# Kernel optimization log

Measured on AMD Instinct MI355X. Metric: run time of the kernel, lower is better.

## Reference

```python
import jax, jax.numpy as jnp
import numpy as np

B, T, J, D = 128, 256, 50, 3
I, H, C = J * D, 1024, 60


def setup_inputs() -> dict:
    key = jax.random.key(0)
    ks = jax.random.split(key, 10)
    s = 0.02
    return {
        "x": jax.random.normal(ks[0], (B, T, J, D), dtype=jnp.float32),
        "h1": jnp.zeros((B, H), jnp.float32),
        "c1": jnp.zeros((B, H), jnp.float32),
        "h2": jnp.zeros((B, H), jnp.float32),
        "c2": jnp.zeros((B, H), jnp.float32),
        "W_ih1": jax.random.normal(ks[1], (4 * H, I), jnp.float32) * s,
        "W_hh1": jax.random.normal(ks[2], (4 * H, H), jnp.float32) * s,
        "b_ih1": jax.random.normal(ks[3], (4 * H,), jnp.float32) * s,
        "b_hh1": jax.random.normal(ks[4], (4 * H,), jnp.float32) * s,
        "W_ih2": jax.random.normal(ks[5], (4 * H, H), jnp.float32) * s,
        "W_hh2": jax.random.normal(ks[6], (4 * H, H), jnp.float32) * s,
        "b_ih2": jax.random.normal(ks[7], (4 * H,), jnp.float32) * s,
        "b_hh2": jax.random.normal(ks[8], (4 * H,), jnp.float32) * s,
        "W_fc": jax.random.normal(ks[9], (C, H), jnp.float32) * s,
        "b_fc": jnp.zeros((C,), jnp.float32),
        "mode": 0,  # 0 == 'val' (no dropout), static
    }


def _lstm_cell(xv, h, c, Wih, Whh, bih, bhh):
    # PyTorch LSTMCell gate order: i, f, g, o
    gates = xv @ Wih.T + bih + h @ Whh.T + bhh  # [B, 4H]
    i, f, g, o = jnp.split(gates, 4, axis=-1)
    c_new = jax.nn.sigmoid(f) * c + jax.nn.sigmoid(i) * jnp.tanh(g)
    h_new = jax.nn.sigmoid(o) * jnp.tanh(c_new)
    return h_new, c_new


def reference(x, h1, c1, h2, c2, W_ih1, W_hh1, b_ih1, b_hh1,
              W_ih2, W_hh2, b_ih2, b_hh2, W_fc, b_fc, mode):
    b, t = x.shape[0], x.shape[1]
    xs = x.reshape(b, t, -1).transpose(1, 0, 2)  # [T, B, I]

    def step(carry, xt):
        h1, c1, h2, c2 = carry
        h1, c1 = _lstm_cell(xt, h1, c1, W_ih1, W_hh1, b_ih1, b_hh1)
        # mode==0 ('val'): no dropout between layers
        h2, c2 = _lstm_cell(h1, h2, c2, W_ih2, W_hh2, b_ih2, b_hh2)
        return (h1, c1, h2, c2), None

    (h1, c1, h2, c2), _ = jax.lax.scan(step, (h1, c1, h2, c2), xs)
    return h2 @ W_fc.T + b_fc  # [B, num_class]
```

## Files before the change

### kernel.cpp

```cpp
#include <hip/hip_runtime.h>
#include <math.h>


typedef __bf16 bf16;
typedef __bf16 bf16x8 __attribute__((ext_vector_type(8)));
typedef float floatx4 __attribute__((ext_vector_type(4)));
typedef unsigned long long ull;

#define B_   128
#define T_   256
#define H_   1024
#define I_   150
#define KX_  160
#define C_   60
#define K1LDS 1280
#define KP    1024
#define K2LDS 2048
#define NLINES 32
#define CSTRIDE 64
#define FLAGLINE 16
#define NCOLS 32
#define NHC  8
#define NT   2

template<int N> struct IC { static constexpr int value = N; };

__device__ __forceinline__ float sigmoidf_(float x) { return 1.f / (1.f + expf(-x)); }

__global__ __launch_bounds__(256)
void convert_all(const float* __restrict__ x,
                 const float* __restrict__ h1in, const float* __restrict__ h2in,
                 bf16* __restrict__ xb, bf16* __restrict__ h1b0, bf16* __restrict__ h2b0,
                 unsigned* __restrict__ cnt)
{
    const size_t nXB = (size_t)T_ * B_ * KX_;
    const size_t nHC = (size_t)B_ * H_;
    size_t idx = (size_t)blockIdx.x * 256 + threadIdx.x;

    if (idx < nXB) {
        size_t t = idx / (B_ * KX_);
        size_t r = idx - t * (B_ * KX_);
        size_t b = r / KX_, k = r - b * KX_;
        xb[idx] = (k < I_) ? (bf16)x[(b * T_ + t) * I_ + k] : (bf16)0.f;
        return;
    }
    idx -= nXB;
    if (idx < nHC) { h1b0[idx] = (bf16)h1in[idx]; return; }
    idx -= nHC;
    if (idx < nHC) { h2b0[idx] = (bf16)h2in[idx]; return; }
    idx -= nHC;
    if (idx < NLINES * CSTRIDE) cnt[idx] = 0u;
}

__global__ __launch_bounds__(512, 2)
void rnn_rebal8(const bf16* __restrict__ xb,
                bf16* __restrict__ h1b0, bf16* __restrict__ h1b1,
                bf16* __restrict__ h2b0, bf16* __restrict__ h2b1,
                float* __restrict__ p0, float* __restrict__ p1,
                const float* __restrict__ c1in, const float* __restrict__ c2in,
                const float* __restrict__ Wih1, const float* __restrict__ Whh1,
                const float* __restrict__ bih1, const float* __restrict__ bhh1,
                const float* __restrict__ Wih2, const float* __restrict__ Whh2,
                const float* __restrict__ bih2, const float* __restrict__ bhh2,
                const float* __restrict__ Wfc, const float* __restrict__ bfc,
                float* __restrict__ out, unsigned* __restrict__ cnt, int nblk)
{
    extern __shared__ bf16 lds[];
    __shared__ __align__(16) bf16 hst[8][16][NHC];

    const int tid   = threadIdx.x;
    const int bid   = blockIdx.x;
    const int layer = (bid >> 3) & 1;
    const int slice = (bid & 7) | ((bid >> 4) << 3);
    const int n0h   = slice * NHC;
    const int arr_per_line = nblk >> 4;
    bf16* ldsP = lds + 32 * K1LDS;

    if (layer == 0) {
        {
            const int cpr = K1LDS >> 3;
            const int total = NCOLS * cpr;
            for (int ci = tid; ci < total; ci += 512) {
                int r = ci / cpr, c = ci - r * cpr;
                int g = r / NHC, j = r - g * NHC;
                int grow = (g << 10) + n0h + j;
                int k0 = c << 3;
                float v[8];
#pragma unroll
                for (int u = 0; u < 8; ++u) {
                    int k = k0 + u;
                    v[u] = (k < I_) ? Wih1[(size_t)grow * I_ + k]
                         : (k < KX_) ? 0.f
                         : (k < KX_ + H_) ? Whh1[(size_t)grow * H_ + (k - KX_)] : 0.f;
                }
                int cs = (c & ~15) | ((c ^ r) & 15);
                bf16* dst = lds + (size_t)r * K1LDS + (cs << 3);
#pragma unroll
                for (int u = 0; u < 8; ++u) dst[u] = (bf16)v[u];
            }
        }
        {
            const int cpr = KP >> 3;
            const int total = NCOLS * cpr;
            for (int ci = tid; ci < total; ci += 512) {
                int r = ci / cpr, c = ci - r * cpr;
                int g = r / NHC, j = r - g * NHC;
                int grow = (g << 10) + n0h + j;
                int k0 = c << 3;
                float v[8];
#pragma unroll
                for (int u = 0; u < 8; ++u) v[u] = Wih2[(size_t)grow * H_ + k0 + u];
                int cs = (c & ~15) | ((c ^ r) & 15);
                bf16* dst = ldsP + (size_t)r * KP + (cs << 3);
#pragma unroll
                for (int u = 0; u < 8; ++u) dst[u] = (bf16)v[u];
            }
        }
    } else {
        const int cpr = KP >> 3;
        const int total = NCOLS * cpr;
        for (int ci = tid; ci < total; ci += 512) {
            int r = ci / cpr, c = ci - r * cpr;
            int g = r / NHC, j = r - g * NHC;
            int grow = (g << 10) + n0h + j;
            int k0 = c << 3;
            float v[8];
#pragma unroll
            for (int u = 0; u < 8; ++u) v[u] = Whh2[(size_t)grow * H_ + k0 + u];
            int cs = (c & ~15) | ((c ^ r) & 15);
            bf16* dst = lds + (size_t)r * KP + (cs << 3);
#pragma unroll
            for (int u = 0; u < 8; ++u) dst[u] = (bf16)v[u];
        }
    }
    __syncthreads();

    const int lane = tid & 63;
    const int wv   = tid >> 6;
    const int jj   = lane & (NHC - 1);
    const int quad = lane >> 4;

    float4 bias;
    {
        const float* bi = layer ? bih2 : bih1;
        const float* bh = layer ? bhh2 : bhh1;
        int col = n0h + jj;
        bias.x = bi[col] + bh[col];
        bias.y = bi[col + H_] + bh[col + H_];
        bias.z = bi[col + 2 * H_] + bh[col + 2 * H_];
        bias.w = bi[col + 3 * H_] + bh[col + 3 * H_];
    }

    float creg[2];
    {
        const float* cin = layer ? c2in : c1in;
        int dup = (lane >> 3) & 1;
#pragma unroll
        for (int rp = 0; rp < 2; ++rp) {
            int row = wv * 16 + quad * 4 + rp * 2 + dup;
            creg[rp] = cin[(size_t)row * H_ + n0h + jj];
        }
    }

    floatx4 acc[NT];
    floatx4 pacc[NT];

    auto seg1 = [&](const bf16* A, int ldA, const bf16* Bb, int ldB,
                    auto nksC, int ksBase) {
        constexpr int NKS = decltype(nksC)::value;
        constexpr int CH  = NKS < 16 ? NKS : 16;
        const int arow = wv * 16 + (lane & 15);
        const bf16* a0 = A + (size_t)arow * ldA + quad * 8;
        for (int blk = 0; blk < NKS; blk += CH) {
            bf16x8 a0r[CH];
#pragma unroll
            for (int i = 0; i < CH; ++i)
                a0r[i] = *(const bf16x8*)(a0 + (blk + i) * 32);
            __builtin_amdgcn_sched_barrier(0);
#pragma unroll
            for (int i = 0; i < CH; ++i) {
                int c = (ksBase + blk + i) * 4 + quad;
#pragma unroll
                for (int t = 0; t < NT; ++t) {
                    int r = t * 16 + (lane & 15);
                    int cs = (c & ~15) | ((c ^ r) & 15);
                    bf16x8 bfr = *(const bf16x8*)(Bb + (size_t)r * ldB + (cs << 3));
                    acc[t] = __builtin_amdgcn_mfma_f32_16x16x32_bf16(a0r[i], bfr, acc[t], 0, 0, 0);
                }
            }
        }
    };

    auto segDual = [&](const bf16* A) {
        const int arow = wv * 16 + (lane & 15);
        const bf16* a0 = A + (size_t)arow * H_ + quad * 8;
        for (int blk = 0; blk < 32; blk += 16) {
            bf16x8 a0r[16];
#pragma unroll
            for (int i = 0; i < 16; ++i)
                a0r[i] = *(const bf16x8*)(a0 + (blk + i) * 32);
            __builtin_amdgcn_sched_barrier(0);
#pragma unroll
            for (int i = 0; i < 16; ++i) {
                int ig = blk + i;
                int c1 = (5 + ig) * 4 + quad;
                int cp = ig * 4 + quad;
#pragma unroll
                for (int t = 0; t < NT; ++t) {
                    int r = t * 16 + (lane & 15);
                    int cs1 = (c1 & ~15) | ((c1 ^ r) & 15);
                    bf16x8 b1 = *(const bf16x8*)(lds + (size_t)r * K1LDS + (cs1 << 3));
                    acc[t] = __builtin_amdgcn_mfma_f32_16x16x32_bf16(a0r[i], b1, acc[t], 0, 0, 0);
                    int csp = (cp & ~15) | ((cp ^ r) & 15);
                    bf16x8 bp = *(const bf16x8*)(ldsP + (size_t)r * KP + (csp << 3));
                    pacc[t] = __builtin_amdgcn_mfma_f32_16x16x32_bf16(a0r[i], bp, pacc[t], 0, 0, 0);
                }
            }
        }
    };

    auto epilogue = [&](bf16* hw) {
        const int base = lane & 48;
#pragma unroll
        for (int r = 0; r < 4; ++r) {
            float vi = __shfl(acc[0][r], base + jj, 64);
            float vf = __shfl(acc[0][r], base + 8 + jj, 64);
            float vg = __shfl(acc[1][r], base + jj, 64);
            float vo = __shfl(acc[1][r], base + 8 + jj, 64);
            bool cond = (((lane >> 3) & 1) == (r & 1));
            int slot = r >> 1;
            if (cond) {
                float cv = creg[slot];
                float cn = sigmoidf_(vf + bias.y) * cv
                         + sigmoidf_(vi + bias.x) * tanhf(vg + bias.z);
                creg[slot] = cn;
                float hn = sigmoidf_(vo + bias.w) * tanhf(cn);
                hst[wv][quad * 4 + r][jj] = (bf16)hn;
            }
        }
        __syncthreads();
        if (lane < 32) {
            int row_l = lane >> 1, cg = lane & 1;
            ull v = *(const ull*)&hst[wv][row_l][cg * 4];
            __hip_atomic_store((ull*)(hw + (size_t)(wv * 16 + row_l) * H_ + n0h + cg * 4),
                               v, __ATOMIC_RELAXED, __HIP_MEMORY_SCOPE_AGENT);
        }
    };

    if (layer == 0) {
#pragma unroll
        for (int t = 0; t < NT; ++t) {
            acc[t]  = (floatx4){0.f, 0.f, 0.f, 0.f};
            pacc[t] = (floatx4){0.f, 0.f, 0.f, 0.f};
        }
        seg1(xb, KX_, lds, K1LDS, IC<5>{}, 0);
    }

    for (int e = 0; e <= T_ + 1; ++e) {
        if (layer == 0 && e <= T_) {
            const bf16* h1r = (e & 1) ? h1b1 : h1b0;
            segDual(h1r);

            float* pw = ((e & 1) ? p1 : p0) + (size_t)slice * B_ * NCOLS;
#pragma unroll
            for (int t = 0; t < NT; ++t)
#pragma unroll
                for (int r = 0; r < 4; ++r) {
                    int row = wv * 16 + quad * 4 + r;
                    __hip_atomic_store(pw + (size_t)row * NCOLS + t * 16 + (lane & 15),
                                       pacc[t][r], __ATOMIC_RELAXED, __HIP_MEMORY_SCOPE_AGENT);
                }

            if (e < T_) {
                bf16* hw = (e & 1) ? h1b0 : h1b1;
                epilogue(hw);
            }
        } else if (layer == 1 && e >= 2) {
#pragma unroll
            for (int t = 0; t < NT; ++t) acc[t] = (floatx4){0.f, 0.f, 0.f, 0.f};

            const float* pr = ((e & 1) ? p0 : p1) + (size_t)slice * B_ * NCOLS;
            float pv[NT][4];
#pragma unroll
            for (int t = 0; t < NT; ++t)
#pragma unroll
                for (int r = 0; r < 4; ++r) {
                    int row = wv * 16 + quad * 4 + r;
                    pv[t][r] = pr[(size_t)row * NCOLS + t * 16 + (lane & 15)];
                }

            const bf16* h2r = (e & 1) ? h2b1 : h2b0;
            seg1(h2r, H_, lds, KP, IC<32>{}, 0);

#pragma unroll
            for (int t = 0; t < NT; ++t)
#pragma unroll
                for (int r = 0; r < 4; ++r) acc[t][r] += pv[t][r];

            bf16* hw = (e & 1) ? h2b0 : h2b1;
            epilogue(hw);
        }

        asm volatile("s_waitcnt vmcnt(0)" ::: "memory");
        __syncthreads();
        const unsigned etag = (unsigned)(e + 1);
        if (tid == 0)
            __hip_atomic_fetch_add(cnt + (bid & 15) * CSTRIDE, 1u,
                                   __ATOMIC_RELAXED, __HIP_MEMORY_SCOPE_AGENT);
        if (layer == 0 && e < T_) {
#pragma unroll
            for (int t = 0; t < NT; ++t) {
                acc[t]  = (floatx4){0.f, 0.f, 0.f, 0.f};
                pacc[t] = (floatx4){0.f, 0.f, 0.f, 0.f};
            }
            if (e + 1 < T_)
                seg1(xb + (size_t)(e + 1) * B_ * KX_, KX_, lds, K1LDS, IC<5>{}, 0);
        }
        if (bid == 0) {
            if (tid < 16) {
                const unsigned tgt = etag * (unsigned)arr_per_line;
                const unsigned* cp = cnt + tid * CSTRIDE;
                while (__hip_atomic_load(cp, __ATOMIC_RELAXED, __HIP_MEMORY_SCOPE_AGENT) < tgt)
                    __builtin_amdgcn_s_sleep(1);
            }
            if (tid == 0)
                __hip_atomic_store(cnt + FLAGLINE * CSTRIDE, etag,
                                   __ATOMIC_RELAXED, __HIP_MEMORY_SCOPE_AGENT);
        } else {
            if (tid == 0) {
                const unsigned* fp = cnt + FLAGLINE * CSTRIDE;
                while (__hip_atomic_load(fp, __ATOMIC_RELAXED, __HIP_MEMORY_SCOPE_AGENT) < etag)
                    __builtin_amdgcn_s_sleep(1);
            }
        }
        __syncthreads();
        if (tid < 64)
            __builtin_amdgcn_fence(__ATOMIC_ACQUIRE, "agent");
        __syncthreads();
    }

    if (bid < B_) {
        const bf16* h2f = h2b0;
        for (int c = wv; c < C_; c += 8) {
            float a = 0.f;
            for (int k = lane; k < H_; k += 64)
                a += (float)h2f[(size_t)bid * H_ + k] * Wfc[(size_t)c * H_ + k];
#pragma unroll
            for (int off = 32; off; off >>= 1) a += __shfl_down(a, off, 64);
            if (lane == 0) out[bid * C_ + c] = a + bfc[c];
        }
    }
}

__global__ __launch_bounds__(512, 2)
void rnn_fallback8(const bf16* __restrict__ xb,
                   bf16* __restrict__ h1b0, bf16* __restrict__ h1b1,
                   bf16* __restrict__ h2b0, bf16* __restrict__ h2b1,
                   float* __restrict__ p0, float* __restrict__ p1,
                   const float* __restrict__ c1in, const float* __restrict__ c2in,
                   const float* __restrict__ Wih1, const float* __restrict__ Whh1,
                   const float* __restrict__ bih1, const float* __restrict__ bhh1,
                   const float* __restrict__ Wih2, const float* __restrict__ Whh2,
                   const float* __restrict__ bih2, const float* __restrict__ bhh2,
                   const float* __restrict__ Wfc, const float* __restrict__ bfc,
                   float* __restrict__ out, unsigned* __restrict__ cnt, int nblk)
{
    extern __shared__ bf16 lds[];
    __shared__ __align__(16) bf16 hst[8][16][NHC];

    const int tid   = threadIdx.x;
    const int bid   = blockIdx.x;
    const int layer = (bid >> 3) & 1;
    const int slice = (bid & 7) | ((bid >> 4) << 3);
    const int n0h   = slice * NHC;
    const int KLDS  = layer ? K2LDS : K1LDS;
    const int arr_per_line = nblk >> 3;

    {
        const int cpr = KLDS >> 3;
        const int total = NCOLS * cpr;
        for (int ci = tid; ci < total; ci += 512) {
            int r = ci / cpr, c = ci - r * cpr;
            int g = r / NHC, j = r - g * NHC;
            int grow = (g << 10) + n0h + j;
            int k0 = c << 3;
            float v[8];
#pragma unroll
            for (int u = 0; u < 8; ++u) {
                int k = k0 + u;
                if (layer == 0)
                    v[u] = (k < I_) ? Wih1[(size_t)grow * I_ + k]
                         : (k < KX_) ? 0.f
                         : (k < KX_ + H_) ? Whh1[(size_t)grow * H_ + (k - KX_)] : 0.f;
                else
                    v[u] = (k < H_) ? Wih2[(size_t)grow * H_ + k]
                                    : Whh2[(size_t)grow * H_ + (k - H_)];
            }
            int cs = (c & ~15) | ((c ^ r) & 15);
            bf16* dst = lds + (size_t)r * KLDS + (cs << 3);
#pragma unroll
            for (int u = 0; u < 8; ++u) dst[u] = (bf16)v[u];
        }
    }
    __syncthreads();

    const int lane = tid & 63;
    const int wv   = tid >> 6;
    const int jj   = lane & (NHC - 1);
    const int quad = lane >> 4;

    float4 bias;
    {
        const float* bi = layer ? bih2 : bih1;
        const float* bh = layer ? bhh2 : bhh1;
        int col = n0h + jj;
        bias.x = bi[col] + bh[col];
        bias.y = bi[col + H_] + bh[col + H_];
        bias.z = bi[col + 2 * H_] + bh[col + 2 * H_];
        bias.w = bi[col + 3 * H_] + bh[col + 3 * H_];
    }

    float creg[2];
    {
        const float* cin = layer ? c2in : c1in;
        int dup = (lane >> 3) & 1;
#pragma unroll
        for (int rp = 0; rp < 2; ++rp) {
            int row = wv * 16 + quad * 4 + rp * 2 + dup;
            creg[rp] = cin[(size_t)row * H_ + n0h + jj];
        }
    }

    floatx4 acc[NT];

    auto seg = [&](const bf16* A, int ldA, auto nksC, int ksBase) {
        constexpr int NKS = decltype(nksC)::value;
        constexpr int CH  = NKS < 16 ? NKS : 16;
        const int arow = wv * 16 + (lane & 15);
        const bf16* a0 = A + (size_t)arow * ldA + quad * 8;
        for (int blk = 0; blk < NKS; blk += CH) {
            bf16x8 a0r[CH];
#pragma unroll
            for (int i = 0; i < CH; ++i)
                a0r[i] = *(const bf16x8*)(a0 + (blk + i) * 32);
            __builtin_amdgcn_sched_barrier(0);
#pragma unroll
            for (int i = 0; i < CH; ++i) {
                int c = (ksBase + blk + i) * 4 + quad;
#pragma unroll
                for (int t = 0; t < NT; ++t) {
                    int r = t * 16 + (lane & 15);
                    int cs = (c & ~15) | ((c ^ r) & 15);
                    bf16x8 bfr = *(const bf16x8*)(lds + (size_t)r * KLDS + (cs << 3));
                    acc[t] = __builtin_amdgcn_mfma_f32_16x16x32_bf16(a0r[i], bfr, acc[t], 0, 0, 0);
                }
            }
        }
    };

    for (int e = 0; e <= T_; ++e) {
        const bool active = layer == 0 ? (e < T_) : (e >= 1);
        if (active) {
#pragma unroll
            for (int t = 0; t < NT; ++t) acc[t] = (floatx4){0.f, 0.f, 0.f, 0.f};

            const bf16* h1r = (e & 1) ? h1b1 : h1b0;
            if (layer == 0) {
                const bf16* xt = xb + (size_t)e * B_ * KX_;
                seg(xt, KX_, IC<5>{}, 0);
                seg(h1r, H_, IC<32>{}, 5);
            } else {
                const bf16* h2r = (e & 1) ? h2b0 : h2b1;
                seg(h1r, H_, IC<32>{}, 0);
                seg(h2r, H_, IC<32>{}, 32);
            }
            bf16* hw = (layer == 0) ? ((e & 1) ? h1b0 : h1b1)
                                    : ((e & 1) ? h2b1 : h2b0);

            const int base = lane & 48;
#pragma unroll
            for (int r = 0; r < 4; ++r) {
                float vi = __shfl(acc[0][r], base + jj, 64);
                float vf = __shfl(acc[0][r], base + 8 + jj, 64);
                float vg = __shfl(acc[1][r], base + jj, 64);
                float vo = __shfl(acc[1][r], base + 8 + jj, 64);
                bool cond = (((lane >> 3) & 1) == (r & 1));
                int slot = r >> 1;
                if (cond) {
                    float cv = creg[slot];
                    float cn = sigmoidf_(vf + bias.y) * cv
                             + sigmoidf_(vi + bias.x) * tanhf(vg + bias.z);
                    creg[slot] = cn;
                    float hn = sigmoidf_(vo + bias.w) * tanhf(cn);
                    hst[wv][quad * 4 + r][jj] = (bf16)hn;
                }
            }
            __syncthreads();
            if (lane < 32) {
                int row_l = lane >> 1, cg = lane & 1;
                ull v = *(const ull*)&hst[wv][row_l][cg * 4];
                __hip_atomic_store((ull*)(hw + (size_t)(wv * 16 + row_l) * H_ + n0h + cg * 4),
                                   v, __ATOMIC_RELAXED, __HIP_MEMORY_SCOPE_AGENT);
            }
        }

        asm volatile("s_waitcnt vmcnt(0)" ::: "memory");
        __syncthreads();
        const unsigned etag = (unsigned)(e + 1);
        if (bid == 0) {
            if (tid == 0)
                __hip_atomic_fetch_add(cnt, 1u, __ATOMIC_RELAXED, __HIP_MEMORY_SCOPE_AGENT);
            if (tid < 8) {
                const unsigned tgt = etag * (unsigned)arr_per_line;
                const unsigned* cp = cnt + tid * CSTRIDE;
                while (__hip_atomic_load(cp, __ATOMIC_RELAXED, __HIP_MEMORY_SCOPE_AGENT) < tgt)
                    __builtin_amdgcn_s_sleep(1);
            }
            if (tid == 0)
                __hip_atomic_store(cnt + 8 * CSTRIDE, etag,
                                   __ATOMIC_RELAXED, __HIP_MEMORY_SCOPE_AGENT);
        } else {
            if (tid == 0) {
                __hip_atomic_fetch_add(cnt + (bid & 7) * CSTRIDE, 1u,
                                       __ATOMIC_RELAXED, __HIP_MEMORY_SCOPE_AGENT);
                const unsigned* fp = cnt + 8 * CSTRIDE;
                while (__hip_atomic_load(fp, __ATOMIC_RELAXED, __HIP_MEMORY_SCOPE_AGENT) < etag)
                    __builtin_amdgcn_s_sleep(1);
            }
        }
        __syncthreads();
        if (tid < 64)
            __builtin_amdgcn_fence(__ATOMIC_ACQUIRE, "agent");
        __syncthreads();
    }

    if (bid < B_) {
        const bf16* h2f = h2b0;
        for (int c = wv; c < C_; c += 8) {
            float a = 0.f;
            for (int k = lane; k < H_; k += 64)
                a += (float)h2f[(size_t)bid * H_ + k] * Wfc[(size_t)c * H_ + k];
#pragma unroll
            for (int off = 32; off; off >>= 1) a += __shfl_down(a, off, 64);
            if (lane == 0) out[bid * C_ + c] = a + bfc[c];
        }
    }
}

extern "C" void kernel_launch(void* const* d_in, const int* in_sizes, int n_in,
                              void* d_out, int out_size, void* d_ws, size_t ws_size,
                              hipStream_t stream)
{
    const float* x    = (const float*)d_in[0];
    const float* h1in = (const float*)d_in[1];
    const float* c1in = (const float*)d_in[2];
    const float* h2in = (const float*)d_in[3];
    const float* c2in = (const float*)d_in[4];
    const float* Wih1 = (const float*)d_in[5];
    const float* Whh1 = (const float*)d_in[6];
    const float* bih1 = (const float*)d_in[7];
    const float* bhh1 = (const float*)d_in[8];
    const float* Wih2 = (const float*)d_in[9];
    const float* Whh2 = (const float*)d_in[10];
    const float* bih2 = (const float*)d_in[11];
    const float* bhh2 = (const float*)d_in[12];
    const float* Wfc  = (const float*)d_in[13];
    const float* bfc  = (const float*)d_in[14];
    float* out = (float*)d_out;

    const size_t szXB  = (size_t)T_ * B_ * KX_ * 2;
    const size_t szH   = (size_t)B_ * H_ * 2;
    const size_t szCnt = (size_t)NLINES * CSTRIDE * 4;
    const size_t szP   = (size_t)128 * B_ * NCOLS * 4;
    const size_t needBase  = szXB + 4 * szH + szCnt;
    const size_t needRebal = needBase + 2 * szP;

    char* p = (char*)d_ws;
    bf16* xb = (bf16*)p;    p += szXB;
    bf16* h1b0 = (bf16*)p;  p += szH;
    bf16* h1b1 = (bf16*)p;  p += szH;
    bf16* h2b0 = (bf16*)p;  p += szH;
    bf16* h2b1 = (bf16*)p;  p += szH;
    unsigned* cnt = (unsigned*)p;  p += szCnt;
    float* p0 = (float*)p;  p += szP;
    float* p1 = (float*)p;

    const size_t citems = (size_t)T_ * B_ * KX_ + 2 * (size_t)B_ * H_ + NLINES * CSTRIDE;
    convert_all<<<(int)((citems + 255) / 256), 256, 0, stream>>>(
        x, h1in, h2in, xb, h1b0, h2b0, cnt);

    int nblk = 256;
    void* args[] = { &xb, &h1b0, &h1b1, &h2b0, &h2b1, &p0, &p1,
                     (void*)&c1in, (void*)&c2in,
                     (void*)&Wih1, (void*)&Whh1, (void*)&bih1, (void*)&bhh1,
                     (void*)&Wih2, (void*)&Whh2, (void*)&bih2, (void*)&bhh2,
                     (void*)&Wfc, (void*)&bfc, &out, &cnt, &nblk };

    hipError_t err = hipErrorOutOfMemory;
    if (ws_size >= needRebal) {
        const unsigned ldsRebal = (unsigned)(32 * K1LDS + 32 * KP) * 2u;
        if (hipFuncSetAttribute((const void*)rnn_rebal8,
                                hipFuncAttributeMaxDynamicSharedMemorySize,
                                (int)ldsRebal) == hipSuccess) {
            err = hipLaunchCooperativeKernel((const void*)rnn_rebal8,
                                             dim3(256), dim3(512), args,
                                             ldsRebal, stream);
        }
    }
    if (err != hipSuccess) {
        (void)hipGetLastError();
        (void)hipFuncSetAttribute((const void*)rnn_fallback8,
                                  hipFuncAttributeMaxDynamicSharedMemorySize, 131072);
        (void)hipLaunchCooperativeKernel((const void*)rnn_fallback8,
                                         dim3(256), dim3(512), args,
                                         131072u, stream);
    }
}
```

Before: 3.548 ms.

## Replace per-step acquire fence with relaxed atomic loads of shared state

Removes the per-timestep agent-scope acquire fence and the extra barrier in the persistent recurrence loop. Instead, cross-block hidden-state and partial-sum reads use relaxed agent-scope atomic loads so they bypass stale caches, with a single fence kept before the final FC. The aim is to cut the cache invalidation and barrier cost on every step of the grid-wide sync. The risk is that 8-byte atomic loads replace 16-byte vector loads, and that ordering now relies on relaxed atomics without an explicit acquire.

```diff
diff --git a/kernel.cpp b/kernel.cpp
--- a/kernel.cpp
+++ b/kernel.cpp
@@ -27,6 +27,15 @@
 
 __device__ __forceinline__ float sigmoidf_(float x) { return 1.f / (1.f + expf(-x)); }
 
+union U16B { ull u[2]; bf16x8 v; };
+
+__device__ __forceinline__ bf16x8 loadH16(const bf16* p) {
+    U16B x;
+    x.u[0] = __hip_atomic_load((const ull*)p,     __ATOMIC_RELAXED, __HIP_MEMORY_SCOPE_AGENT);
+    x.u[1] = __hip_atomic_load((const ull*)p + 1, __ATOMIC_RELAXED, __HIP_MEMORY_SCOPE_AGENT);
+    return x.v;
+}
+
 __global__ __launch_bounds__(256)
 void convert_all(const float* __restrict__ x,
                  const float* __restrict__ h1in, const float* __restrict__ h2in,
@@ -165,26 +174,44 @@
     floatx4 acc[NT];
     floatx4 pacc[NT];
 
-    auto seg1 = [&](const bf16* A, int ldA, const bf16* Bb, int ldB,
-                    auto nksC, int ksBase) {
-        constexpr int NKS = decltype(nksC)::value;
-        constexpr int CH  = NKS < 16 ? NKS : 16;
+    auto segX = [&](const bf16* A) {
         const int arow = wv * 16 + (lane & 15);
-        const bf16* a0 = A + (size_t)arow * ldA + quad * 8;
-        for (int blk = 0; blk < NKS; blk += CH) {
-            bf16x8 a0r[CH];
-#pragma unroll
-            for (int i = 0; i < CH; ++i)
-                a0r[i] = *(const bf16x8*)(a0 + (blk + i) * 32);
+        const bf16* a0 = A + (size_t)arow * KX_ + quad * 8;
+        bf16x8 a0r[5];
+#pragma unroll
+        for (int i = 0; i < 5; ++i)
+            a0r[i] = *(const bf16x8*)(a0 + i * 32);
+        __builtin_amdgcn_sched_barrier(0);
+#pragma unroll
+        for (int i = 0; i < 5; ++i) {
+            int c = i * 4 + quad;
+#pragma unroll
+            for (int t = 0; t < NT; ++t) {
+                int r = t * 16 + (lane & 15);
+                int cs = (c & ~15) | ((c ^ r) & 15);
+                bf16x8 bfr = *(const bf16x8*)(lds + (size_t)r * K1LDS + (cs << 3));
+                acc[t] = __builtin_amdgcn_mfma_f32_16x16x32_bf16(a0r[i], bfr, acc[t], 0, 0, 0);
+            }
+        }
+    };
+
+    auto segH2 = [&](const bf16* A) {
+        const int arow = wv * 16 + (lane & 15);
+        const bf16* a0 = A + (size_t)arow * H_ + quad * 8;
+        for (int blk = 0; blk < 32; blk += 16) {
+            bf16x8 a0r[16];
+#pragma unroll
+            for (int i = 0; i < 16; ++i)
+                a0r[i] = loadH16(a0 + (blk + i) * 32);
             __builtin_amdgcn_sched_barrier(0);
 #pragma unroll
-            for (int i = 0; i < CH; ++i) {
-                int c = (ksBase + blk + i) * 4 + quad;
+            for (int i = 0; i < 16; ++i) {
+                int c = (blk + i) * 4 + quad;
 #pragma unroll
                 for (int t = 0; t < NT; ++t) {
                     int r = t * 16 + (lane & 15);
                     int cs = (c & ~15) | ((c ^ r) & 15);
-                    bf16x8 bfr = *(const bf16x8*)(Bb + (size_t)r * ldB + (cs << 3));
+                    bf16x8 bfr = *(const bf16x8*)(lds + (size_t)r * KP + (cs << 3));
                     acc[t] = __builtin_amdgcn_mfma_f32_16x16x32_bf16(a0r[i], bfr, acc[t], 0, 0, 0);
                 }
             }
@@ -198,7 +225,7 @@
             bf16x8 a0r[16];
 #pragma unroll
             for (int i = 0; i < 16; ++i)
-                a0r[i] = *(const bf16x8*)(a0 + (blk + i) * 32);
+                a0r[i] = loadH16(a0 + (blk + i) * 32);
             __builtin_amdgcn_sched_barrier(0);
 #pragma unroll
             for (int i = 0; i < 16; ++i) {
@@ -253,7 +280,7 @@
             acc[t]  = (floatx4){0.f, 0.f, 0.f, 0.f};
             pacc[t] = (floatx4){0.f, 0.f, 0.f, 0.f};
         }
-        seg1(xb, KX_, lds, K1LDS, IC<5>{}, 0);
+        segX(xb);
     }
 
     for (int e = 0; e <= T_ + 1; ++e) {
@@ -286,11 +313,12 @@
 #pragma unroll
                 for (int r = 0; r < 4; ++r) {
                     int row = wv * 16 + quad * 4 + r;
-                    pv[t][r] = pr[(size_t)row * NCOLS + t * 16 + (lane & 15)];
+                    pv[t][r] = __hip_atomic_load(pr + (size_t)row * NCOLS + t * 16 + (lane & 15),
+                                                 __ATOMIC_RELAXED, __HIP_MEMORY_SCOPE_AGENT);
                 }
 
             const bf16* h2r = (e & 1) ? h2b1 : h2b0;
-            seg1(h2r, H_, lds, KP, IC<32>{}, 0);
+            segH2(h2r);
 
 #pragma unroll
             for (int t = 0; t < NT; ++t)
@@ -314,7 +342,7 @@
                 pacc[t] = (floatx4){0.f, 0.f, 0.f, 0.f};
             }
             if (e + 1 < T_)
-                seg1(xb + (size_t)(e + 1) * B_ * KX_, KX_, lds, K1LDS, IC<5>{}, 0);
+                segX(xb + (size_t)(e + 1) * B_ * KX_);
         }
         if (bid == 0) {
             if (tid < 16) {
@@ -334,10 +362,11 @@
             }
         }
         __syncthreads();
-        if (tid < 64)
-            __builtin_amdgcn_fence(__ATOMIC_ACQUIRE, "agent");
-        __syncthreads();
-    }
+    }
+
+    if (tid < 64)
+        __builtin_amdgcn_fence(__ATOMIC_ACQUIRE, "agent");
+    __syncthreads();
 
     if (bid < B_) {
         const bf16* h2f = h2b0;
```

Result: slower. 4.864 ms (+37.1%).

## Decouple layer barriers with per-layer flags and triple-buffered partials

Applied to the files above, without the earlier changes.

Adds a new persistent kernel in which layer-0 and layer-1 blocks synchronize through separate barrier flags instead of one global barrier each step. The partial-product buffer becomes triple-buffered, so layer 0 can run up to two steps ahead of layer 1, and layer-1 blocks wait only on their own layer plus layer 0's progress. This is meant to shrink the critical path of the grid-wide barrier and let the layers overlap. In exchange it needs more workspace and more complex cross-layer dependency logic, and it drops the old fallback kernel.

```diff
diff --git a/kernel.cpp b/kernel.cpp
--- a/kernel.cpp
+++ b/kernel.cpp
@@ -15,10 +15,11 @@
 #define C_   60
 #define K1LDS 1280
 #define KP    1024
-#define K2LDS 2048
-#define NLINES 32
+#define NLINES 40
 #define CSTRIDE 64
 #define FLAGLINE 16
+#define L0FLAG 32
+#define L1FLAG 33
 #define NCOLS 32
 #define NHC  8
 #define NT   2
@@ -50,6 +51,353 @@
     if (idx < nHC) { h2b0[idx] = (bf16)h2in[idx]; return; }
     idx -= nHC;
     if (idx < NLINES * CSTRIDE) cnt[idx] = 0u;
+}
+
+__device__ __forceinline__ void stage_rebal(
+    bf16* lds, bf16* ldsP, int tid, int layer, int n0h,
+    const float* Wih1, const float* Whh1, const float* Wih2, const float* Whh2)
+{
+    if (layer == 0) {
+        {
+            const int cpr = K1LDS >> 3;
+            const int total = NCOLS * cpr;
+            for (int ci = tid; ci < total; ci += 512) {
+                int r = ci / cpr, c = ci - r * cpr;
+                int g = r / NHC, j = r - g * NHC;
+                int grow = (g << 10) + n0h + j;
+                int k0 = c << 3;
+                float v[8];
+#pragma unroll
+                for (int u = 0; u < 8; ++u) {
+                    int k = k0 + u;
+                    v[u] = (k < I_) ? Wih1[(size_t)grow * I_ + k]
+                         : (k < KX_) ? 0.f
+                         : (k < KX_ + H_) ? Whh1[(size_t)grow * H_ + (k - KX_)] : 0.f;
+                }
+                int cs = (c & ~15) | ((c ^ r) & 15);
+                bf16* dst = lds + (size_t)r * K1LDS + (cs << 3);
+#pragma unroll
+                for (int u = 0; u < 8; ++u) dst[u] = (bf16)v[u];
+            }
+        }
+        {
+            const int cpr = KP >> 3;
+            const int total = NCOLS * cpr;
+            for (int ci = tid; ci < total; ci += 512) {
+                int r = ci / cpr, c = ci - r * cpr;
+                int g = r / NHC, j = r - g * NHC;
+                int grow = (g << 10) + n0h + j;
+                int k0 = c << 3;
+                float v[8];
+#pragma unroll
+                for (int u = 0; u < 8; ++u) v[u] = Wih2[(size_t)grow * H_ + k0 + u];
+                int cs = (c & ~15) | ((c ^ r) & 15);
+                bf16* dst = ldsP + (size_t)r * KP + (cs << 3);
+#pragma unroll
+                for (int u = 0; u < 8; ++u) dst[u] = (bf16)v[u];
+            }
+        }
+    } else {
+        const int cpr = KP >> 3;
+        const int total = NCOLS * cpr;
+        for (int ci = tid; ci < total; ci += 512) {
+            int r = ci / cpr, c = ci - r * cpr;
+            int g = r / NHC, j = r - g * NHC;
+            int grow = (g << 10) + n0h + j;
+            int k0 = c << 3;
+            float v[8];
+#pragma unroll
+            for (int u = 0; u < 8; ++u) v[u] = Whh2[(size_t)grow * H_ + k0 + u];
+            int cs = (c & ~15) | ((c ^ r) & 15);
+            bf16* dst = lds + (size_t)r * KP + (cs << 3);
+#pragma unroll
+            for (int u = 0; u < 8; ++u) dst[u] = (bf16)v[u];
+        }
+    }
+}
+
+__global__ __launch_bounds__(512, 2)
+void rnn_decoup8(const bf16* __restrict__ xb,
+                 bf16* __restrict__ h1b0, bf16* __restrict__ h1b1,
+                 bf16* __restrict__ h2b0, bf16* __restrict__ h2b1,
+                 float* __restrict__ p0, float* __restrict__ p1, float* __restrict__ p2,
+                 const float* __restrict__ c1in, const float* __restrict__ c2in,
+                 const float* __restrict__ Wih1, const float* __restrict__ Whh1,
+                 const float* __restrict__ bih1, const float* __restrict__ bhh1,
+                 const float* __restrict__ Wih2, const float* __restrict__ Whh2,
+                 const float* __restrict__ bih2, const float* __restrict__ bhh2,
+                 const float* __restrict__ Wfc, const float* __restrict__ bfc,
+                 float* __restrict__ out, unsigned* __restrict__ cnt, int nblk)
+{
+    extern __shared__ bf16 lds[];
+    __shared__ __align__(16) bf16 hst[8][16][NHC];
+
+    const int tid   = threadIdx.x;
+    const int bid   = blockIdx.x;
+    const int layer = (bid >> 3) & 1;
+    const int slice = (bid & 7) | ((bid >> 4) << 3);
+    const int n0h   = slice * NHC;
+    const int line  = layer * 16 + ((bid & 7) | (((bid >> 4) & 1) << 3));
+    bf16* ldsP = lds + 32 * K1LDS;
+
+    stage_rebal(lds, ldsP, tid, layer, n0h, Wih1, Whh1, Wih2, Whh2);
+    __syncthreads();
+
+    const int lane = tid & 63;
+    const int wv   = tid >> 6;
+    const int jj   = lane & (NHC - 1);
+    const int quad = lane >> 4;
+
+    float4 bias;
+    {
+        const float* bi = layer ? bih2 : bih1;
+        const float* bh = layer ? bhh2 : bhh1;
+        int col = n0h + jj;
+        bias.x = bi[col] + bh[col];
+        bias.y = bi[col + H_] + bh[col + H_];
+        bias.z = bi[col + 2 * H_] + bh[col + 2 * H_];
+        bias.w = bi[col + 3 * H_] + bh[col + 3 * H_];
+    }
+
+    float creg[2];
+    {
+        const float* cin = layer ? c2in : c1in;
+        int dup = (lane >> 3) & 1;
+#pragma unroll
+        for (int rp = 0; rp < 2; ++rp) {
+            int row = wv * 16 + quad * 4 + rp * 2 + dup;
+            creg[rp] = cin[(size_t)row * H_ + n0h + jj];
+        }
+    }
+
+    floatx4 acc[NT];
+    floatx4 pacc[NT];
+
+    auto seg1 = [&](const bf16* A, int ldA, const bf16* Bb, int ldB,
+                    auto nksC, int ksBase) {
+        constexpr int NKS = decltype(nksC)::value;
+        constexpr int CH  = NKS < 16 ? NKS : 16;
+        const int arow = wv * 16 + (lane & 15);
+        const bf16* a0 = A + (size_t)arow * ldA + quad * 8;
+        for (int blk = 0; blk < NKS; blk += CH) {
+            bf16x8 a0r[CH];
+#pragma unroll
+            for (int i = 0; i < CH; ++i)
+                a0r[i] = *(const bf16x8*)(a0 + (blk + i) * 32);
+            __builtin_amdgcn_sched_barrier(0);
+#pragma unroll
+            for (int i = 0; i < CH; ++i) {
+                int c = (ksBase + blk + i) * 4 + quad;
+#pragma unroll
+                for (int t = 0; t < NT; ++t) {
+                    int r = t * 16 + (lane & 15);
+                    int cs = (c & ~15) | ((c ^ r) & 15);
+                    bf16x8 bfr = *(const bf16x8*)(Bb + (size_t)r * ldB + (cs << 3));
+                    acc[t] = __builtin_amdgcn_mfma_f32_16x16x32_bf16(a0r[i], bfr, acc[t], 0, 0, 0);
+                }
+            }
+        }
+    };
+
+    auto segDual = [&](const bf16* A) {
+        const int arow = wv * 16 + (lane & 15);
+        const bf16* a0 = A + (size_t)arow * H_ + quad * 8;
+        for (int blk = 0; blk < 32; blk += 16) {
+            bf16x8 a0r[16];
+#pragma unroll
+            for (int i = 0; i < 16; ++i)
+                a0r[i] = *(const bf16x8*)(a0 + (blk + i) * 32);
+            __builtin_amdgcn_sched_barrier(0);
+#pragma unroll
+            for (int i = 0; i < 16; ++i) {
+                int ig = blk + i;
+                int c1 = (5 + ig) * 4 + quad;
+                int cp = ig * 4 + quad;
+#pragma unroll
+                for (int t = 0; t < NT; ++t) {
+                    int r = t * 16 + (lane & 15);
+                    int cs1 = (c1 & ~15) | ((c1 ^ r) & 15);
+                    bf16x8 b1 = *(const bf16x8*)(lds + (size_t)r * K1LDS + (cs1 << 3));
+                    acc[t] = __builtin_amdgcn_mfma_f32_16x16x32_bf16(a0r[i], b1, acc[t], 0, 0, 0);
+                    int csp = (cp & ~15) | ((cp ^ r) & 15);
+                    bf16x8 bp = *(const bf16x8*)(ldsP + (size_t)r * KP + (csp << 3));
+                    pacc[t] = __builtin_amdgcn_mfma_f32_16x16x32_bf16(a0r[i], bp, pacc[t], 0, 0, 0);
+                }
+            }
+        }
+    };
+
+    auto epilogue = [&](bf16* hw) {
+        const int base = lane & 48;
+#pragma unroll
+        for (int r = 0; r < 4; ++r) {
+            float vi = __shfl(acc[0][r], base + jj, 64);
+            float vf = __shfl(acc[0][r], base + 8 + jj, 64);
+            float vg = __shfl(acc[1][r], base + jj, 64);
+            float vo = __shfl(acc[1][r], base + 8 + jj, 64);
+            bool cond = (((lane >> 3) & 1) == (r & 1));
+            int slot = r >> 1;
+            if (cond) {
+                float cv = creg[slot];
+                float cn = sigmoidf_(vf + bias.y) * cv
+                         + sigmoidf_(vi + bias.x) * tanhf(vg + bias.z);
+                creg[slot] = cn;
+                float hn = sigmoidf_(vo + bias.w) * tanhf(cn);
+                hst[wv][quad * 4 + r][jj] = (bf16)hn;
+            }
+        }
+        __syncthreads();
+        if (lane < 32) {
+            int row_l = lane >> 1, cg = lane & 1;
+            ull v = *(const ull*)&hst[wv][row_l][cg * 4];
+            __hip_atomic_store((ull*)(hw + (size_t)(wv * 16 + row_l) * H_ + n0h + cg * 4),
+                               v, __ATOMIC_RELAXED, __HIP_MEMORY_SCOPE_AGENT);
+        }
+    };
+
+    if (layer == 0) {
+#pragma unroll
+        for (int t = 0; t < NT; ++t) {
+            acc[t]  = (floatx4){0.f, 0.f, 0.f, 0.f};
+            pacc[t] = (floatx4){0.f, 0.f, 0.f, 0.f};
+        }
+        seg1(xb, KX_, lds, K1LDS, IC<5>{}, 0);
+    }
+
+    for (int e = 0; e <= T_ + 1; ++e) {
+        const int pm  = e % 3;
+        const int pmr = (e + 2) % 3;
+        float* const pbuf[3] = { p0, p1, p2 };
+
+        if (layer == 0 && e <= T_) {
+            const bf16* h1r = (e & 1) ? h1b1 : h1b0;
+            segDual(h1r);
+
+            float* pw = pbuf[pm] + (size_t)slice * B_ * NCOLS;
+#pragma unroll
+            for (int t = 0; t < NT; ++t)
+#pragma unroll
+                for (int r = 0; r < 4; ++r) {
+                    int row = wv * 16 + quad * 4 + r;
+                    __hip_atomic_store(pw + (size_t)row * NCOLS + t * 16 + (lane & 15),
+                                       pacc[t][r], __ATOMIC_RELAXED, __HIP_MEMORY_SCOPE_AGENT);
+                }
+
+            if (e < T_) {
+                bf16* hw = (e & 1) ? h1b0 : h1b1;
+                epilogue(hw);
+            }
+        } else if (layer == 1 && e >= 2) {
+#pragma unroll
+            for (int t = 0; t < NT; ++t) acc[t] = (floatx4){0.f, 0.f, 0.f, 0.f};
+
+            const float* pr = pbuf[pmr] + (size_t)slice * B_ * NCOLS;
+            float pv[NT][4];
+#pragma unroll
+            for (int t = 0; t < NT; ++t)
+#pragma unroll
+                for (int r = 0; r < 4; ++r) {
+                    int row = wv * 16 + quad * 4 + r;
+                    pv[t][r] = pr[(size_t)row * NCOLS + t * 16 + (lane & 15)];
+                }
+
+            const bf16* h2r = (e & 1) ? h2b1 : h2b0;
+            seg1(h2r, H_, lds, KP, IC<32>{}, 0);
+
+#pragma unroll
+            for (int t = 0; t < NT; ++t)
+#pragma unroll
+                for (int r = 0; r < 4; ++r) acc[t][r] += pv[t][r];
+
+            bf16* hw = (e & 1) ? h2b0 : h2b1;
+            epilogue(hw);
+        }
+
+        asm volatile("s_waitcnt vmcnt(0)" ::: "memory");
+        __syncthreads();
+        const int etag = e + 1;
+        if (tid == 0)
+            __hip_atomic_fetch_add(cnt + line * CSTRIDE, 1u,
+                                   __ATOMIC_RELAXED, __HIP_MEMORY_SCOPE_AGENT);
+        if (layer == 0 && e < T_) {
+#pragma unroll
+            for (int t = 0; t < NT; ++t) {
+                acc[t]  = (floatx4){0.f, 0.f, 0.f, 0.f};
+                pacc[t] = (floatx4){0.f, 0.f, 0.f, 0.f};
+            }
+            if (e + 1 < T_)
+                seg1(xb + (size_t)(e + 1) * B_ * KX_, KX_, lds, K1LDS, IC<5>{}, 0);
+        }
+        if (layer == 0) {
+            if (bid == 0) {
+                if (tid < 16) {
+                    const unsigned tgt = 8u * (unsigned)etag;
+                    const unsigned* cp = cnt + tid * CSTRIDE;
+                    while (__hip_atomic_load(cp, __ATOMIC_RELAXED, __HIP_MEMORY_SCOPE_AGENT) < tgt)
+                        __builtin_amdgcn_s_sleep(1);
+                }
+                if (tid == 0)
+                    __hip_atomic_store(cnt + L0FLAG * CSTRIDE, (unsigned)etag,
+                                       __ATOMIC_RELAXED, __HIP_MEMORY_SCOPE_AGENT);
+            } else if (tid == 0) {
+                const unsigned* fp = cnt + L0FLAG * CSTRIDE;
+                while (__hip_atomic_load(fp, __ATOMIC_RELAXED, __HIP_MEMORY_SCOPE_AGENT) < (unsigned)etag)
+                    __builtin_amdgcn_s_sleep(1);
+            }
+            if (tid == 0 && etag >= 3) {
+                const unsigned* fp = cnt + L1FLAG * CSTRIDE;
+                while (__hip_atomic_load(fp, __ATOMIC_RELAXED, __HIP_MEMORY_SCOPE_AGENT) < (unsigned)(etag - 2))
+                    __builtin_amdgcn_s_sleep(1);
+            }
+        } else {
+            if (bid == 8) {
+                if (tid < 16) {
+                    const unsigned tgt = 8u * (unsigned)etag;
+                    const unsigned* cp = cnt + (16 + tid) * CSTRIDE;
+                    while (__hip_atomic_load(cp, __ATOMIC_RELAXED, __HIP_MEMORY_SCOPE_AGENT) < tgt)
+                        __builtin_amdgcn_s_sleep(1);
+                }
+                if (tid == 0)
+                    __hip_atomic_store(cnt + L1FLAG * CSTRIDE, (unsigned)etag,
+                                       __ATOMIC_RELAXED, __HIP_MEMORY_SCOPE_AGENT);
+            } else if (tid == 0) {
+                const unsigned* fp = cnt + L1FLAG * CSTRIDE;
+                while (__hip_atomic_load(fp, __ATOMIC_RELAXED, __HIP_MEMORY_SCOPE_AGENT) < (unsigned)etag)
+                    __builtin_amdgcn_s_sleep(1);
+            }
+            if (tid == 0) {
+                const unsigned* fp = cnt + L0FLAG * CSTRIDE;
+                while (__hip_atomic_load(fp, __ATOMIC_RELAXED, __HIP_MEMORY_SCOPE_AGENT) < (unsigned)etag)
+                    __builtin_amdgcn_s_sleep(1);
+            }
+        }
+        __syncthreads();
+        if (tid < 64)
+            __builtin_amdgcn_fence(__ATOMIC_ACQUIRE, "agent");
+        __syncthreads();
+    }
+
+    if (tid == 0 && layer == 0) {
+        const unsigned* fp = cnt + L1FLAG * CSTRIDE;
+        while (__hip_atomic_load(fp, __ATOMIC_RELAXED, __HIP_MEMORY_SCOPE_AGENT) < (unsigned)(T_ + 2))
+            __builtin_amdgcn_s_sleep(1);
+    }
+    __syncthreads();
+    if (tid < 64)
+        __builtin_amdgcn_fence(__ATOMIC_ACQUIRE, "agent");
+    __syncthreads();
+
+    if (bid < B_) {
+        const bf16* h2f = h2b0;
+        for (int c = wv; c < C_; c += 8) {
+            float a = 0.f;
+            for (int k = lane; k < H_; k += 64)
+                a += (float)h2f[(size_t)bid * H_ + k] * Wfc[(size_t)c * H_ + k];
+#pragma unroll
+            for (int off = 32; off; off >>= 1) a += __shfl_down(a, off, 64);
+            if (lane == 0) out[bid * C_ + c] = a + bfc[c];
+        }
+    }
 }
 
 __global__ __launch_bounds__(512, 2)
@@ -76,63 +424,7 @@
     const int arr_per_line = nblk >> 4;
     bf16* ldsP = lds + 32 * K1LDS;
 
-    if (layer == 0) {
-        {
-            const int cpr = K1LDS >> 3;
-            const int total = NCOLS * cpr;
-            for (int ci = tid; ci < total; ci += 512) {
-                int r = ci / cpr, c = ci - r * cpr;
-                int g = r / NHC, j = r - g * NHC;
-                int grow = (g << 10) + n0h + j;
-                int k0 = c << 3;
-                float v[8];
-#pragma unroll
-                for (int u = 0; u < 8; ++u) {
-                    int k = k0 + u;
-                    v[u] = (k < I_) ? Wih1[(size_t)grow * I_ + k]
-                         : (k < KX_) ? 0.f
-                         : (k < KX_ + H_) ? Whh1[(size_t)grow * H_ + (k - KX_)] : 0.f;
-                }
-                int cs = (c & ~15) | ((c ^ r) & 15);
-                bf16* dst = lds + (size_t)r * K1LDS + (cs << 3);
-#pragma unroll
-                for (int u = 0; u < 8; ++u) dst[u] = (bf16)v[u];
-            }
-        }
-        {
-            const int cpr = KP >> 3;
-            const int total = NCOLS * cpr;
-            for (int ci = tid; ci < total; ci += 512) {
-                int r = ci / cpr, c = ci - r * cpr;
-                int g = r / NHC, j = r - g * NHC;
-                int grow = (g << 10) + n0h + j;
-                int k0 = c << 3;
-                float v[8];
-#pragma unroll
-                for (int u = 0; u < 8; ++u) v[u] = Wih2[(size_t)grow * H_ + k0 + u];
-                int cs = (c & ~15) | ((c ^ r) & 15);
-                bf16* dst = ldsP + (size_t)r * KP + (cs << 3);
-#pragma unroll
-                for (int u = 0; u < 8; ++u) dst[u] = (bf16)v[u];
-            }
-        }
-    } else {
-        const int cpr = KP >> 3;
-        const int total = NCOLS * cpr;
-        for (int ci = tid; ci < total; ci += 512) {
-            int r = ci / cpr, c = ci - r * cpr;
-            int g = r / NHC, j = r - g * NHC;
-            int grow = (g << 10) + n0h + j;
-            int k0 = c << 3;
-            float v[8];
-#pragma unroll
-            for (int u = 0; u < 8; ++u) v[u] = Whh2[(size_t)grow * H_ + k0 + u];
-            int cs = (c & ~15) | ((c ^ r) & 15);
-            bf16* dst = lds + (size_t)r * KP + (cs << 3);
-#pragma unroll
-            for (int u = 0; u < 8; ++u) dst[u] = (bf16)v[u];
-        }
-    }
+    stage_rebal(lds, ldsP, tid, layer, n0h, Wih1, Whh1, Wih2, Whh2);
     __syncthreads();
 
     const int lane = tid & 63;
@@ -329,201 +621,6 @@
         } else {
             if (tid == 0) {
                 const unsigned* fp = cnt + FLAGLINE * CSTRIDE;
-                while (__hip_atomic_load(fp, __ATOMIC_RELAXED, __HIP_MEMORY_SCOPE_AGENT) < etag)
-                    __builtin_amdgcn_s_sleep(1);
-            }
-        }
-        __syncthreads();
-        if (tid < 64)
-            __builtin_amdgcn_fence(__ATOMIC_ACQUIRE, "agent");
-        __syncthreads();
-    }
-
-    if (bid < B_) {
-        const bf16* h2f = h2b0;
-        for (int c = wv; c < C_; c += 8) {
-            float a = 0.f;
-            for (int k = lane; k < H_; k += 64)
-                a += (float)h2f[(size_t)bid * H_ + k] * Wfc[(size_t)c * H_ + k];
-#pragma unroll
-            for (int off = 32; off; off >>= 1) a += __shfl_down(a, off, 64);
-            if (lane == 0) out[bid * C_ + c] = a + bfc[c];
-        }
-    }
-}
-
-__global__ __launch_bounds__(512, 2)
-void rnn_fallback8(const bf16* __restrict__ xb,
-                   bf16* __restrict__ h1b0, bf16* __restrict__ h1b1,
-                   bf16* __restrict__ h2b0, bf16* __restrict__ h2b1,
-                   float* __restrict__ p0, float* __restrict__ p1,
-                   const float* __restrict__ c1in, const float* __restrict__ c2in,
-                   const float* __restrict__ Wih1, const float* __restrict__ Whh1,
-                   const float* __restrict__ bih1, const float* __restrict__ bhh1,
-                   const float* __restrict__ Wih2, const float* __restrict__ Whh2,
-                   const float* __restrict__ bih2, const float* __restrict__ bhh2,
-                   const float* __restrict__ Wfc, const float* __restrict__ bfc,
-                   float* __restrict__ out, unsigned* __restrict__ cnt, int nblk)
-{
-    extern __shared__ bf16 lds[];
-    __shared__ __align__(16) bf16 hst[8][16][NHC];
-
-    const int tid   = threadIdx.x;
-    const int bid   = blockIdx.x;
-    const int layer = (bid >> 3) & 1;
-    const int slice = (bid & 7) | ((bid >> 4) << 3);
-    const int n0h   = slice * NHC;
-    const int KLDS  = layer ? K2LDS : K1LDS;
-    const int arr_per_line = nblk >> 3;
-
-    {
-        const int cpr = KLDS >> 3;
-        const int total = NCOLS * cpr;
-        for (int ci = tid; ci < total; ci += 512) {
-            int r = ci / cpr, c = ci - r * cpr;
-            int g = r / NHC, j = r - g * NHC;
-            int grow = (g << 10) + n0h + j;
-            int k0 = c << 3;
-            float v[8];
-#pragma unroll
-            for (int u = 0; u < 8; ++u) {
-                int k = k0 + u;
-                if (layer == 0)
-                    v[u] = (k < I_) ? Wih1[(size_t)grow * I_ + k]
-                         : (k < KX_) ? 0.f
-                         : (k < KX_ + H_) ? Whh1[(size_t)grow * H_ + (k - KX_)] : 0.f;
-                else
-                    v[u] = (k < H_) ? Wih2[(size_t)grow * H_ + k]
-                                    : Whh2[(size_t)grow * H_ + (k - H_)];
-            }
-            int cs = (c & ~15) | ((c ^ r) & 15);
-            bf16* dst = lds + (size_t)r * KLDS + (cs << 3);
-#pragma unroll
-            for (int u = 0; u < 8; ++u) dst[u] = (bf16)v[u];
-        }
-    }
-    __syncthreads();
-
-    const int lane = tid & 63;
-    const int wv   = tid >> 6;
-    const int jj   = lane & (NHC - 1);
-    const int quad = lane >> 4;
-
-    float4 bias;
-    {
-        const float* bi = layer ? bih2 : bih1;
-        const float* bh = layer ? bhh2 : bhh1;
-        int col = n0h + jj;
-        bias.x = bi[col] + bh[col];
-        bias.y = bi[col + H_] + bh[col + H_];
-        bias.z = bi[col + 2 * H_] + bh[col + 2 * H_];
-        bias.w = bi[col + 3 * H_] + bh[col + 3 * H_];
-    }
-
-    float creg[2];
-    {
-        const float* cin = layer ? c2in : c1in;
-        int dup = (lane >> 3) & 1;
-#pragma unroll
-        for (int rp = 0; rp < 2; ++rp) {
-            int row = wv * 16 + quad * 4 + rp * 2 + dup;
-            creg[rp] = cin[(size_t)row * H_ + n0h + jj];
-        }
-    }
-
-    floatx4 acc[NT];
-
-    auto seg = [&](const bf16* A, int ldA, auto nksC, int ksBase) {
-        constexpr int NKS = decltype(nksC)::value;
-        constexpr int CH  = NKS < 16 ? NKS : 16;
-        const int arow = wv * 16 + (lane & 15);
-        const bf16* a0 = A + (size_t)arow * ldA + quad * 8;
-        for (int blk = 0; blk < NKS; blk += CH) {
-            bf16x8 a0r[CH];
-#pragma unroll
-            for (int i = 0; i < CH; ++i)
-                a0r[i] = *(const bf16x8*)(a0 + (blk + i) * 32);
-            __builtin_amdgcn_sched_barrier(0);
-#pragma unroll
-            for (int i = 0; i < CH; ++i) {
-                int c = (ksBase + blk + i) * 4 + quad;
-#pragma unroll
-                for (int t = 0; t < NT; ++t) {
-                    int r = t * 16 + (lane & 15);
-                    int cs = (c & ~15) | ((c ^ r) & 15);
-                    bf16x8 bfr = *(const bf16x8*)(lds + (size_t)r * KLDS + (cs << 3));
-                    acc[t] = __builtin_amdgcn_mfma_f32_16x16x32_bf16(a0r[i], bfr, acc[t], 0, 0, 0);
-                }
-            }
-        }
-    };
-
-    for (int e = 0; e <= T_; ++e) {
-        const bool active = layer == 0 ? (e < T_) : (e >= 1);
-        if (active) {
-#pragma unroll
-            for (int t = 0; t < NT; ++t) acc[t] = (floatx4){0.f, 0.f, 0.f, 0.f};
-
-            const bf16* h1r = (e & 1) ? h1b1 : h1b0;
-            if (layer == 0) {
-                const bf16* xt = xb + (size_t)e * B_ * KX_;
-                seg(xt, KX_, IC<5>{}, 0);
-                seg(h1r, H_, IC<32>{}, 5);
-            } else {
-                const bf16* h2r = (e & 1) ? h2b0 : h2b1;
-                seg(h1r, H_, IC<32>{}, 0);
-                seg(h2r, H_, IC<32>{}, 32);
-            }
-            bf16* hw = (layer == 0) ? ((e & 1) ? h1b0 : h1b1)
-                                    : ((e & 1) ? h2b1 : h2b0);
-
-            const int base = lane & 48;
-#pragma unroll
-            for (int r = 0; r < 4; ++r) {
-                float vi = __shfl(acc[0][r], base + jj, 64);
-                float vf = __shfl(acc[0][r], base + 8 + jj, 64);
-                float vg = __shfl(acc[1][r], base + jj, 64);
-                float vo = __shfl(acc[1][r], base + 8 + jj, 64);
-                bool cond = (((lane >> 3) & 1) == (r & 1));
-                int slot = r >> 1;
-                if (cond) {
-                    float cv = creg[slot];
-                    float cn = sigmoidf_(vf + bias.y) * cv
-                             + sigmoidf_(vi + bias.x) * tanhf(vg + bias.z);
-                    creg[slot] = cn;
-                    float hn = sigmoidf_(vo + bias.w) * tanhf(cn);
-                    hst[wv][quad * 4 + r][jj] = (bf16)hn;
-                }
-            }
-            __syncthreads();
-            if (lane < 32) {
-                int row_l = lane >> 1, cg = lane & 1;
-                ull v = *(const ull*)&hst[wv][row_l][cg * 4];
-                __hip_atomic_store((ull*)(hw + (size_t)(wv * 16 + row_l) * H_ + n0h + cg * 4),
-                                   v, __ATOMIC_RELAXED, __HIP_MEMORY_SCOPE_AGENT);
-            }
-        }
-
-        asm volatile("s_waitcnt vmcnt(0)" ::: "memory");
-        __syncthreads();
-        const unsigned etag = (unsigned)(e + 1);
-        if (bid == 0) {
-            if (tid == 0)
-                __hip_atomic_fetch_add(cnt, 1u, __ATOMIC_RELAXED, __HIP_MEMORY_SCOPE_AGENT);
-            if (tid < 8) {
-                const unsigned tgt = etag * (unsigned)arr_per_line;
-                const unsigned* cp = cnt + tid * CSTRIDE;
-                while (__hip_atomic_load(cp, __ATOMIC_RELAXED, __HIP_MEMORY_SCOPE_AGENT) < tgt)
-                    __builtin_amdgcn_s_sleep(1);
-            }
-            if (tid == 0)
-                __hip_atomic_store(cnt + 8 * CSTRIDE, etag,
-                                   __ATOMIC_RELAXED, __HIP_MEMORY_SCOPE_AGENT);
-        } else {
-            if (tid == 0) {
-                __hip_atomic_fetch_add(cnt + (bid & 7) * CSTRIDE, 1u,
-                                       __ATOMIC_RELAXED, __HIP_MEMORY_SCOPE_AGENT);
-                const unsigned* fp = cnt + 8 * CSTRIDE;
                 while (__hip_atomic_load(fp, __ATOMIC_RELAXED, __HIP_MEMORY_SCOPE_AGENT) < etag)
                     __builtin_amdgcn_s_sleep(1);
             }
@@ -572,8 +669,8 @@
     const size_t szH   = (size_t)B_ * H_ * 2;
     const size_t szCnt = (size_t)NLINES * CSTRIDE * 4;
     const size_t szP   = (size_t)128 * B_ * NCOLS * 4;
-    const size_t needBase  = szXB + 4 * szH + szCnt;
-    const size_t needRebal = needBase + 2 * szP;
+    const size_t needR13 = szXB + 4 * szH + szCnt + 2 * szP;
+    const size_t needDec = szXB + 4 * szH + szCnt + 3 * szP;
 
     char* p = (char*)d_ws;
     bf16* xb = (bf16*)p;    p += szXB;
@@ -583,36 +680,44 @@
     bf16* h2b1 = (bf16*)p;  p += szH;
     unsigned* cnt = (unsigned*)p;  p += szCnt;
     float* p0 = (float*)p;  p += szP;
-    float* p1 = (float*)p;
+    float* p1 = (float*)p;  p += szP;
+    float* p2 = (float*)p;
 
     const size_t citems = (size_t)T_ * B_ * KX_ + 2 * (size_t)B_ * H_ + NLINES * CSTRIDE;
     convert_all<<<(int)((citems + 255) / 256), 256, 0, stream>>>(
         x, h1in, h2in, xb, h1b0, h2b0, cnt);
 
     int nblk = 256;
-    void* args[] = { &xb, &h1b0, &h1b1, &h2b0, &h2b1, &p0, &p1,
-                     (void*)&c1in, (void*)&c2in,
-                     (void*)&Wih1, (void*)&Whh1, (void*)&bih1, (void*)&bhh1,
-                     (void*)&Wih2, (void*)&Whh2, (void*)&bih2, (void*)&bhh2,
-                     (void*)&Wfc, (void*)&bfc, &out, &cnt, &nblk };
-
+    void* argsDec[] = { &xb, &h1b0, &h1b1, &h2b0, &h2b1, &p0, &p1, &p2,
+                        (void*)&c1in, (void*)&c2in,
+                        (void*)&Wih1, (void*)&Whh1, (void*)&bih1, (void*)&bhh1,
+                        (void*)&Wih2, (void*)&Whh2, (void*)&bih2, (void*)&bhh2,
+                        (void*)&Wfc, (void*)&bfc, &out, &cnt, &nblk };
+    void* argsR13[] = { &xb, &h1b0, &h1b1, &h2b0, &h2b1, &p0, &p1,
+                        (void*)&c1in, (void*)&c2in,
+                        (void*)&Wih1, (void*)&Whh1, (void*)&bih1, (void*)&bhh1,
+                        (void*)&Wih2, (void*)&Whh2, (void*)&bih2, (void*)&bhh2,
+                        (void*)&Wfc, (void*)&bfc, &out, &cnt, &nblk };
+
+    const unsigned ldsRebal = (unsigned)(32 * K1LDS + 32 * KP) * 2u;
     hipError_t err = hipErrorOutOfMemory;
-    if (ws_size >= needRebal) {
-        const unsigned ldsRebal = (unsigned)(32 * K1LDS + 32 * KP) * 2u;
+    if (ws_size >= needDec) {
+        if (hipFuncSetAttribute((const void*)rnn_decoup8,
+                                hipFuncAttributeMaxDynamicSharedMemorySize,
+                                (int)ldsRebal) == hipSuccess) {
+            err = hipLaunchCooperativeKernel((const void*)rnn_decoup8,
+                                             dim3(256), dim3(512), argsDec,
+                                             ldsRebal, stream);
+        }
+    }
+    if (err != hipSuccess && ws_size >= needR13) {
+        (void)hipGetLastError();
         if (hipFuncSetAttribute((const void*)rnn_rebal8,
                                 hipFuncAttributeMaxDynamicSharedMemorySize,
                                 (int)ldsRebal) == hipSuccess) {
-            err = hipLaunchCooperativeKernel((const void*)rnn_rebal8,
-                                             dim3(256), dim3(512), args,
+            (void)hipLaunchCooperativeKernel((const void*)rnn_rebal8,
+                                             dim3(256), dim3(512), argsR13,
                                              ldsRebal, stream);
         }
     }
-    if (err != hipSuccess) {
-        (void)hipGetLastError();
-        (void)hipFuncSetAttribute((const void*)rnn_fallback8,
-                                  hipFuncAttributeMaxDynamicSharedMemorySize, 131072);
-        (void)hipLaunchCooperativeKernel((const void*)rnn_fallback8,
-                                         dim3(256), dim3(512), args,
-                                         131072u, stream);
-    }
 }
```

Result: faster. 3.330 ms (-6.2%).
